# Kernel tuning notes

Measured on AMD Instinct MI355X. Metric: run time of the kernel, lower is better.

The kernel has to match this reference:

```python
import jax, jax.numpy as jnp
import numpy as np

D_MODEL = 512
N_HEADS = 8
D_K = D_MODEL // N_HEADS


def setup_inputs() -> dict:
    key = jax.random.key(0)
    ks = jax.random.split(key, 12)
    B, L = 2, 512
    s = 1.0 / np.sqrt(D_MODEL)
    sk = 1.0 / np.sqrt(D_K)
    return {
        "query": jax.random.normal(ks[0], (B, L, D_MODEL), jnp.float32),
        "key": jax.random.normal(ks[1], (B, L, D_MODEL), jnp.float32),
        "value": jax.random.normal(ks[2], (B, L, D_MODEL), jnp.float32),
        "Wq": jax.random.normal(ks[3], (D_MODEL, D_MODEL), jnp.float32) * s,
        "bq": jnp.zeros((D_MODEL,), jnp.float32),
        "Wk": jax.random.normal(ks[4], (D_MODEL, D_MODEL), jnp.float32) * s,
        "bk": jnp.zeros((D_MODEL,), jnp.float32),
        "Wv": jax.random.normal(ks[5], (D_MODEL, D_MODEL), jnp.float32) * s,
        "bv": jnp.zeros((D_MODEL,), jnp.float32),
        "Wo": jax.random.normal(ks[6], (D_MODEL, D_MODEL), jnp.float32) * s,
        "bo": jnp.zeros((D_MODEL,), jnp.float32),
        "Aq": jax.random.normal(ks[7], (D_K, D_K), jnp.float32) * sk,  # inner W_q (no bias)
        "Ak": jax.random.normal(ks[8], (D_K, D_K), jnp.float32) * sk,  # inner W_k (no bias)
        "av": jax.random.normal(ks[9], (D_K,), jnp.float32) * sk,      # inner v (d_k -> 1)
    }


def _split_heads(x):
    B, L, _ = x.shape
    return x.reshape(B, L, N_HEADS, D_K).transpose(0, 2, 1, 3)  # [B,H,L,dk]


def reference(query, key, value, Wq, bq, Wk, bk, Wv, bv, Wo, bo, Aq, Ak, av):
    # outer projections (torch Linear: x @ W.T + b)
    Q = _split_heads(query @ Wq.T + bq)   # [B,H,Lq,dk]
    K = _split_heads(key @ Wk.T + bk)     # [B,H,Lk,dk]
    V = _split_heads(value @ Wv.T + bv)   # [B,H,Lk,dk]
    # inner additive attention: e_ij = v^T tanh(Aq q_i + Ak k_j)
    qp = Q @ Aq.T                          # [B,H,Lq,dk]
    kp = K @ Ak.T                          # [B,H,Lk,dk]
    energy = jnp.tanh(qp[:, :, :, None, :] + kp[:, :, None, :, :])  # [B,H,Lq,Lk,dk]
    scores = jnp.einsum('bhqkd,d->bhqk', energy, av)
    attn = jax.nn.softmax(scores, axis=-1)  # dropout disabled (eval)
    out = jnp.einsum('bhqk,bhkd->bhqd', attn, V)  # [B,H,Lq,dk]
    B, _, Lq, _ = out.shape
    out = out.transpose(0, 2, 1, 3).reshape(B, Lq, D_MODEL)
    return out @ Wo.T + bo
```

## Files before the change

### kernel.cpp

```cpp
#include <hip/hip_runtime.h>

#define LOG2E 1.4426950408889634f

typedef __bf16 bf16x8 __attribute__((ext_vector_type(8)));
typedef float f32x4 __attribute__((ext_vector_type(4)));
typedef float f32x2 __attribute__((ext_vector_type(2)));
typedef unsigned short u16x8 __attribute__((ext_vector_type(8)));

__device__ __forceinline__ unsigned short bfb(__bf16 b){
  union { __bf16 b; unsigned short u; } z; z.b = b; return z.u;
}


__global__ __launch_bounds__(256) void prep_all(
    const float* __restrict__ Wq, const float* __restrict__ Aq,
    const float* __restrict__ Wk, const float* __restrict__ Ak,
    const float* __restrict__ bq, const float* __restrict__ bk,
    const float* __restrict__ av,
    const float* __restrict__ Wv, const float* __restrict__ Wo,
    const float* __restrict__ Qin, const float* __restrict__ Kin,
    const float* __restrict__ Vin,
    unsigned short* __restrict__ W2qp, unsigned short* __restrict__ W2kp,
    unsigned short* __restrict__ Wvp,  unsigned short* __restrict__ Wop,
    unsigned short* __restrict__ qhi, unsigned short* __restrict__ qlo,
    unsigned short* __restrict__ khi, unsigned short* __restrict__ klo,
    unsigned short* __restrict__ vhi, unsigned short* __restrict__ vlo,
    float* __restrict__ b2q, float* __restrict__ b2k, float* __restrict__ av2g){
  if (blockIdx.x >= 513){
    if (blockIdx.y) return;
    int j = blockIdx.x - 513;
    const float* src; unsigned short *dh, *dl;
    if (j < 256){ src = Qin; dh = qhi; dl = qlo; }
    else if (j < 512){ src = Kin; dh = khi; dl = klo; j -= 256; }
    else { src = Vin; dh = vhi; dl = vlo; j -= 512; }
    int base = (j * 256 + threadIdx.x) * 8;
    f32x4 v0 = *(const f32x4*)(src + base);
    f32x4 v1 = *(const f32x4*)(src + base + 4);
    u16x8 hh, ll;
    #pragma unroll
    for (int t = 0; t < 8; t++){
      float f = (t < 4) ? v0[t] : v1[t - 4];
      __bf16 hb = (__bf16)f;
      hh[t] = bfb(hb);
      ll[t] = bfb((__bf16)(f - (float)hb));
    }
    *(u16x8*)(dh + base) = hh;
    *(u16x8*)(dl + base) = ll;
    return;
  }
  if (blockIdx.x >= 256){
    if (blockIdx.x == 512){
      if (blockIdx.y == 0){
        #pragma unroll
        for (int rep = 0; rep < 2; rep++){
          int n = rep * 256 + threadIdx.x;
          int h = n >> 6, e = n & 63;
          float aq = 0.f, ak = 0.f;
          for (int c = 0; c < 64; c++){
            aq += Aq[e*64 + c] * bq[h*64 + c];
            ak += Ak[e*64 + c] * bk[h*64 + c];
          }
          b2q[n] = aq * (2.f * LOG2E);
          b2k[n] = ak * (2.f * LOG2E);
        }
      } else {
        if (threadIdx.x < 64) av2g[threadIdx.x] = -2.f * LOG2E * av[threadIdx.x];
      }
      return;
    }
    const float* src = blockIdx.y ? Wo : Wv;
    unsigned short* dst = blockIdx.y ? Wop : Wvp;
    int base = ((blockIdx.x - 256) * 256 + threadIdx.x) * 4;
    int n = base >> 9, k0 = base & 511;
    float4 v = *(const float4*)(src + base);
    ushort4 h, l;
    float f; __bf16 hb;
    f = v.x; hb = (__bf16)f; h.x = bfb(hb); l.x = bfb((__bf16)(f - (float)hb));
    f = v.y; hb = (__bf16)f; h.y = bfb(hb); l.y = bfb((__bf16)(f - (float)hb));
    f = v.z; hb = (__bf16)f; h.z = bfb(hb); l.z = bfb((__bf16)(f - (float)hb));
    f = v.w; hb = (__bf16)f; h.w = bfb(hb); l.w = bfb((__bf16)(f - (float)hb));
    int nt = n >> 4, ln = n & 15;
    int ks = k0 >> 5, q = (k0 & 31) >> 3, j0 = k0 & 7;
    size_t off = (size_t)((nt*16 + ks) * 2) * 512 + (q*16 + ln) * 8 + j0;
    *(ushort4*)(dst + off)       = h;
    *(ushort4*)(dst + off + 512) = l;
    return;
  }
  const float* W  = blockIdx.y ? Wk : Wq;
  const float* Am = blockIdx.y ? Ak : Aq;
  unsigned short* dst = blockIdx.y ? W2kp : W2qp;
  int idx = blockIdx.x * 256 + threadIdx.x;
  int n = idx >> 7;
  int k0 = (idx & 127) * 4;
  int h = n >> 6, e = n & 63;
  float4 acc = {0.f, 0.f, 0.f, 0.f};
  #pragma unroll 8
  for (int c = 0; c < 64; c++){
    float am = Am[e*64 + c];
    float4 wv = *(const float4*)(W + (size_t)(h*64 + c)*512 + k0);
    acc.x += am * wv.x;
    acc.y += am * wv.y;
    acc.z += am * wv.z;
    acc.w += am * wv.w;
  }
  int nt = n >> 4, ln = n & 15;
  int ks = k0 >> 5, q = (k0 & 31) >> 3, j0 = k0 & 7;
  size_t off = (size_t)((nt*16 + ks) * 2) * 512 + (q*16 + ln) * 8 + j0;
  ushort4 hh, ll;
  float f; __bf16 hb;
  f = acc.x * (2.f * LOG2E); hb = (__bf16)f; hh.x = bfb(hb); ll.x = bfb((__bf16)(f - (float)hb));
  f = acc.y * (2.f * LOG2E); hb = (__bf16)f; hh.y = bfb(hb); ll.y = bfb((__bf16)(f - (float)hb));
  f = acc.z * (2.f * LOG2E); hb = (__bf16)f; hh.z = bfb(hb); ll.z = bfb((__bf16)(f - (float)hb));
  f = acc.w * (2.f * LOG2E); hb = (__bf16)f; hh.w = bfb(hb); ll.w = bfb((__bf16)(f - (float)hb));
  *(ushort4*)(dst + off)       = hh;
  *(ushort4*)(dst + off + 512) = ll;
}

struct GemmBatch {
  const unsigned short* Ahi;
  const unsigned short* Alo;
  const unsigned short* Bp;
  const float* bias;
  float* Cf;
  int transposed;
  int expout;
};
struct GemmArgs { GemmBatch g[3]; };

__global__ __launch_bounds__(256) void gemm_nk(GemmArgs ga){
  GemmBatch gb = ga.g[blockIdx.z];
  __shared__ unsigned short AhiS[32 * 72];
  __shared__ unsigned short AloS[32 * 72];
  const int tid = threadIdx.x, lane = tid & 63, w = tid >> 6;
  const int l15 = lane & 15, quad = lane >> 4;
  const int m0  = blockIdx.x * 32;
  const int nt0 = blockIdx.y * 4;
  const int wr = w >> 1, wc = w & 1;
  f32x4 ac0 = {0.f,0.f,0.f,0.f}, ac1 = ac0;

  const int srow = tid >> 3;
  const int scol = (tid & 7) * 8;
  const unsigned short* srcH = gb.Ahi + (size_t)(m0 + srow) * 512 + scol;
  const unsigned short* srcL = gb.Alo + (size_t)(m0 + srow) * 512 + scol;
  unsigned short* dstH = &AhiS[srow * 72 + scol];
  unsigned short* dstL = &AloS[srow * 72 + scol];
  u16x8 ph = *(const u16x8*)srcH;
  u16x8 pl = *(const u16x8*)srcL;

  const int arow = (wr * 16 + l15) * 72;

  for (int kc = 0; kc < 8; kc++){
    __syncthreads();
    *(u16x8*)dstH = ph;
    *(u16x8*)dstL = pl;
    if (kc < 7){
      ph = *(const u16x8*)(srcH + (kc + 1) * 64);
      pl = *(const u16x8*)(srcL + (kc + 1) * 64);
    }
    __syncthreads();
    #pragma unroll
    for (int s = 0; s < 2; s++){
      int ks = kc * 2 + s;
      bf16x8 ah = *(const bf16x8*)&AhiS[arow + s*32 + quad*8];
      bf16x8 al = *(const bf16x8*)&AloS[arow + s*32 + quad*8];
      #pragma unroll
      for (int t = 0; t < 2; t++){
        int nt = nt0 + wc*2 + t;
        const unsigned short* bp = gb.Bp + (size_t)((nt*16 + ks) * 2) * 512 + lane*8;
        bf16x8 bh = *(const bf16x8*)bp;
        bf16x8 bl = *(const bf16x8*)(bp + 512);
        f32x4& ac = t ? ac1 : ac0;
        ac = __builtin_amdgcn_mfma_f32_16x16x32_bf16(ah, bh, ac, 0, 0, 0);
        ac = __builtin_amdgcn_mfma_f32_16x16x32_bf16(al, bh, ac, 0, 0, 0);
        ac = __builtin_amdgcn_mfma_f32_16x16x32_bf16(ah, bl, ac, 0, 0, 0);
      }
    }
  }

  const int mrow = m0 + wr * 16 + quad * 4;
  #pragma unroll
  for (int t = 0; t < 2; t++){
    f32x4 v = t ? ac1 : ac0;
    int n = nt0*16 + wc*32 + t*16 + l15;
    float bs = gb.bias[n];
    #pragma unroll
    for (int r = 0; r < 4; r++){
      float val = v[r] + bs;
      if (gb.expout) val = __builtin_amdgcn_exp2f(val);
      int m2 = mrow + r;
      if (gb.transposed){
        gb.Cf[(size_t)(((m2 >> 9) * 8 + (n >> 6)) * 512 + (m2 & 511)) * 64 + (n & 63)] = val;
      } else {
        gb.Cf[(size_t)m2 * 512 + n] = val;
      }
    }
  }
}

__global__ __launch_bounds__(1024, 8) void attn_kernel(
    const float* __restrict__ eqQ, const float* __restrict__ ekp,
    const float* __restrict__ Vv, const float* __restrict__ av2g,
    unsigned short* __restrict__ Ohhi, unsigned short* __restrict__ Ohlo){
  __shared__ float bufA[64 * 130];
  __shared__ float bufB[64 * 130];
  __shared__ unsigned short pcb[2 * 16 * 136];
  __shared__ float dn[16];
  __shared__ float eqs[16 * 64];
  __shared__ float avs[64];
  float* cmb = bufA;

  const int tid = threadIdx.x, lane = tid & 63, w = tid >> 6;
  const int l15 = lane & 15, quad = lane >> 4;
  const int bh = blockIdx.y;
  const int i0 = blockIdx.x * 16;
  const size_t kbase = (size_t)(bh >> 3) * 512 * 512 + (size_t)(bh & 7) * 64;
  const int r0 = __builtin_amdgcn_readfirstlane(w);
  const int ntile = w & 3, kq = w >> 2;

  float den = 0.f;
  f32x4 Cacc = {0.f, 0.f, 0.f, 0.f};

  {
    eqs[w * 64 + lane] = eqQ[((size_t)bh * 512 + i0 + w) * 64 + lane];
    if (w == 0) avs[lane] = av2g[lane];
    #pragma unroll
    for (int m = 0; m < 4; m++){
      int i = w + 16 * m;
      float a = ekp[kbase + (size_t)(2*i    ) * 512 + lane];
      float b = ekp[kbase + (size_t)(2*i + 1) * 512 + lane];
      *(float2*)&bufA[lane * 130 + 2*i] = make_float2(a, b);
    }
  }
  __syncthreads();

  for (int c = 0; c < 4; c++){
    float va[4], vb[4], ka[4], kb[4];
    #pragma unroll
    for (int m = 0; m < 4; m++){
      int i = w + 16 * m;
      va[m] = Vv[kbase + (size_t)(c*128 + 2*i    ) * 512 + lane];
      vb[m] = Vv[kbase + (size_t)(c*128 + 2*i + 1) * 512 + lane];
    }
    if (c < 3){
      #pragma unroll
      for (int m = 0; m < 4; m++){
        int i = w + 16 * m;
        ka[m] = ekp[kbase + (size_t)((c+1)*128 + 2*i    ) * 512 + lane];
        kb[m] = ekp[kbase + (size_t)((c+1)*128 + 2*i + 1) * 512 + lane];
      }
    }
    f32x2 sacc = {0.f, 0.f};
    #pragma unroll 4
    for (int d = 0; d < 64; d += 4){
      f32x4 eq4 = *(const f32x4*)&eqs[r0 * 64 + d];
      f32x4 a4  = *(const f32x4*)&avs[d];
      f32x2 ek0 = *(const f32x2*)&bufA[(d  ) * 130 + 2 * lane];
      f32x2 ek1 = *(const f32x2*)&bufA[(d+1) * 130 + 2 * lane];
      f32x2 ek2 = *(const f32x2*)&bufA[(d+2) * 130 + 2 * lane];
      f32x2 ek3 = *(const f32x2*)&bufA[(d+3) * 130 + 2 * lane];
      f32x2 A = __builtin_elementwise_fma((f32x2){eq4[0], eq4[0]}, ek0, (f32x2){1.f, 1.f});
      f32x2 B = __builtin_elementwise_fma((f32x2){eq4[1], eq4[1]}, ek1, (f32x2){1.f, 1.f});
      f32x2 t = __builtin_elementwise_fma((f32x2){a4[1], a4[1]}, A, (f32x2){a4[0], a4[0]} * B);
      f32x2 dpr = A * B;
      f32x2 r;
      r.x = __builtin_amdgcn_rcpf(dpr.x);
      r.y = __builtin_amdgcn_rcpf(dpr.y);
      sacc = __builtin_elementwise_fma(t, r, sacc);
      f32x2 C = __builtin_elementwise_fma((f32x2){eq4[2], eq4[2]}, ek2, (f32x2){1.f, 1.f});
      f32x2 D = __builtin_elementwise_fma((f32x2){eq4[3], eq4[3]}, ek3, (f32x2){1.f, 1.f});
      f32x2 t2 = __builtin_elementwise_fma((f32x2){a4[3], a4[3]}, C, (f32x2){a4[2], a4[2]} * D);
      f32x2 dpr2 = C * D;
      f32x2 r2;
      r2.x = __builtin_amdgcn_rcpf(dpr2.x);
      r2.y = __builtin_amdgcn_rcpf(dpr2.y);
      sacc = __builtin_elementwise_fma(t2, r2, sacc);
    }
    float e0 = __builtin_amdgcn_exp2f(sacc.x);
    float e1 = __builtin_amdgcn_exp2f(sacc.y);
    den += e0 + e1;
    {
      __bf16 h0 = (__bf16)e0, h1 = (__bf16)e1;
      ushort2 hi = { bfb(h0), bfb(h1) };
      ushort2 lo = { bfb((__bf16)(e0 - (float)h0)), bfb((__bf16)(e1 - (float)h1)) };
      *(ushort2*)&pcb[(0*16 + r0) * 136 + 2*lane] = hi;
      *(ushort2*)&pcb[(1*16 + r0) * 136 + 2*lane] = lo;
    }
    #pragma unroll
    for (int m = 0; m < 4; m++){
      int i = w + 16 * m;
      *(float2*)&bufB[lane * 130 + 2*i] = make_float2(va[m], vb[m]);
    }
    __syncthreads();

    {
      int k0 = kq * 32 + quad * 8;
      bf16x8 ph = *(const bf16x8*)&pcb[(0*16 + l15) * 136 + k0];
      bf16x8 pl = *(const bf16x8*)&pcb[(1*16 + l15) * 136 + k0];
      const float* vp = &bufB[(ntile*16 + l15) * 130 + k0];
      bf16x8 vh, vl;
      #pragma unroll
      for (int j = 0; j < 8; j++){
        float f = vp[j];
        __bf16 h = (__bf16)f;
        vh[j] = h; vl[j] = (__bf16)(f - (float)h);
      }
      Cacc = __builtin_amdgcn_mfma_f32_16x16x32_bf16(ph, vh, Cacc, 0, 0, 0);
      Cacc = __builtin_amdgcn_mfma_f32_16x16x32_bf16(pl, vh, Cacc, 0, 0, 0);
      Cacc = __builtin_amdgcn_mfma_f32_16x16x32_bf16(ph, vl, Cacc, 0, 0, 0);
    }
    if (c < 3){
      #pragma unroll
      for (int m = 0; m < 4; m++){
        int i = w + 16 * m;
        *(float2*)&bufA[lane * 130 + 2*i] = make_float2(ka[m], kb[m]);
      }
    }
    __syncthreads();
  }

  #pragma unroll
  for (int off = 1; off < 64; off <<= 1)
    den += __shfl_xor(den, off, 64);
  if (lane == 0) dn[r0] = den;
  if (kq > 0){
    #pragma unroll
    for (int r = 0; r < 4; r++) cmb[(w - 4) * 256 + lane * 4 + r] = Cacc[r];
  }
  __syncthreads();
  if (kq == 0){
    #pragma unroll
    for (int r = 0; r < 4; r++){
      float cv = Cacc[r];
      #pragma unroll
      for (int j = 0; j < 3; j++) cv += cmb[(j*4 + ntile) * 256 + lane * 4 + r];
      int row = quad * 4 + r;
      int d = ntile * 16 + l15;
      float val = cv / dn[row];
      __bf16 hb = (__bf16)val;
      size_t oi = kbase + (size_t)(i0 + row) * 512 + d;
      Ohhi[oi] = bfb(hb);
      Ohlo[oi] = bfb((__bf16)(val - (float)hb));
    }
  }
}

extern "C" void kernel_launch(void* const* d_in, const int* in_sizes, int n_in,
                              void* d_out, int out_size, void* d_ws, size_t ws_size,
                              hipStream_t stream){
  const float* q_in = (const float*)d_in[0];
  const float* k_in = (const float*)d_in[1];
  const float* v_in = (const float*)d_in[2];
  const float* Wq_  = (const float*)d_in[3];
  const float* bq_  = (const float*)d_in[4];
  const float* Wk_  = (const float*)d_in[5];
  const float* bk_  = (const float*)d_in[6];
  const float* Wv_  = (const float*)d_in[7];
  const float* bv_  = (const float*)d_in[8];
  const float* Wo_  = (const float*)d_in[9];
  const float* bo_  = (const float*)d_in[10];
  const float* Aq_  = (const float*)d_in[11];
  const float* Ak_  = (const float*)d_in[12];
  const float* av_  = (const float*)d_in[13];

  char* ws = (char*)d_ws;
  unsigned short* W2qp = (unsigned short*)(ws + 0);
  unsigned short* W2kp = (unsigned short*)(ws + 1048576);
  unsigned short* Ohhi = (unsigned short*)(ws + 0);
  unsigned short* Ohlo = (unsigned short*)(ws + 1048576);
  unsigned short* Wvp  = (unsigned short*)(ws + 2097152);
  unsigned short* Wop  = (unsigned short*)(ws + 3145728);
  float* b2q  = (float*)(ws + 4194304);
  float* b2k  = (float*)(ws + 4196352);
  float* av2g = (float*)(ws + 4198400);
  float* eqQ  = (float*)(ws + 4198656);
  float* ekp  = (float*)(ws + 6295808);
  float* Vw   = (float*)(ws + 8392960);
  unsigned short* qhi = (unsigned short*)(ws + 10490112);
  unsigned short* qlo = (unsigned short*)(ws + 11538688);
  unsigned short* khi = (unsigned short*)(ws + 12587264);
  unsigned short* klo = (unsigned short*)(ws + 13635840);
  unsigned short* vhi = (unsigned short*)(ws + 14684416);
  unsigned short* vlo = (unsigned short*)(ws + 15732992);

  prep_all<<<dim3(1281, 2, 1), 256, 0, stream>>>(Wq_, Aq_, Wk_, Ak_, bq_, bk_, av_,
                                                 Wv_, Wo_, q_in, k_in, v_in,
                                                 W2qp, W2kp, Wvp, Wop,
                                                 qhi, qlo, khi, klo, vhi, vlo,
                                                 b2q, b2k, av2g);

  GemmArgs ga;
  ga.g[0] = { qhi, qlo, W2qp, b2q, eqQ, 1, 1 };
  ga.g[1] = { khi, klo, W2kp, b2k, ekp, 0, 1 };
  ga.g[2] = { vhi, vlo, Wvp,  bv_, Vw,  0, 0 };
  gemm_nk<<<dim3(32, 8, 3), 256, 0, stream>>>(ga);

  attn_kernel<<<dim3(32, 16, 1), 1024, 0, stream>>>(eqQ, ekp, Vw, av2g, Ohhi, Ohlo);

  GemmArgs go;
  go.g[0] = { Ohhi, Ohlo, Wop, bo_, (float*)d_out, 0, 0 };
  go.g[1] = go.g[0];
  go.g[2] = go.g[0];
  gemm_nk<<<dim3(32, 8, 1), 256, 0, stream>>>(go);
}
```

Baseline: 151.8 us.

## Split attention over key blocks with atomic accumulation and register-tiled scores

Replaces the single-pass attention kernel (one block of 1024 threads per 16 query rows, looping over all keys) with a split-K kernel. Each 256-thread block handles 64 queries by 128 keys and keeps 16 query rows per wave in registers, so each key element loaded from shared memory is reused across rows. Partial P·V results and softmax denominators are accumulated into global buffers with atomicAdd, and a new finish kernel normalises the output and converts it to split bf16. The V projection GEMM now writes V pre-transposed and pre-split into bf16 hi/lo, and prep_all zeroes the accumulators. This adds an extra launch and atomic traffic, and the summation order is no longer deterministic.

```diff
diff --git a/kernel.cpp b/kernel.cpp
--- a/kernel.cpp
+++ b/kernel.cpp
@@ -25,9 +25,19 @@
     unsigned short* __restrict__ qhi, unsigned short* __restrict__ qlo,
     unsigned short* __restrict__ khi, unsigned short* __restrict__ klo,
     unsigned short* __restrict__ vhi, unsigned short* __restrict__ vlo,
-    float* __restrict__ b2q, float* __restrict__ b2k, float* __restrict__ av2g){
+    float* __restrict__ b2q, float* __restrict__ b2k, float* __restrict__ av2g,
+    float* __restrict__ zbase){
   if (blockIdx.x >= 513){
-    if (blockIdx.y) return;
+    if (blockIdx.y){
+      int x = blockIdx.x - 513;
+      if (x < 260){
+        float* z = zbase + (size_t)(x * 256 + threadIdx.x) * 8;
+        f32x4 zz = {0.f, 0.f, 0.f, 0.f};
+        *(f32x4*)z = zz;
+        *(f32x4*)(z + 4) = zz;
+      }
+      return;
+    }
     int j = blockIdx.x - 513;
     const float* src; unsigned short *dh, *dl;
     if (j < 256){ src = Qin; dh = qhi; dl = qlo; }
@@ -122,8 +132,11 @@
   const unsigned short* Bp;
   const float* bias;
   float* Cf;
+  unsigned short* Chi;
+  unsigned short* Clo;
   int transposed;
   int expout;
+  int dual;
 };
 struct GemmArgs { GemmBatch g[3]; };
 
@@ -188,7 +201,12 @@
       float val = v[r] + bs;
       if (gb.expout) val = __builtin_amdgcn_exp2f(val);
       int m2 = mrow + r;
-      if (gb.transposed){
+      if (gb.dual){
+        size_t o = (size_t)(((m2 >> 9) * 8 + (n >> 6)) * 64 + (n & 63)) * 512 + (m2 & 511);
+        __bf16 hb = (__bf16)val;
+        gb.Chi[o] = bfb(hb);
+        gb.Clo[o] = bfb((__bf16)(val - (float)hb));
+      } else if (gb.transposed){
         gb.Cf[(size_t)(((m2 >> 9) * 8 + (n >> 6)) * 512 + (m2 & 511)) * 64 + (n & 63)] = val;
       } else {
         gb.Cf[(size_t)m2 * 512 + n] = val;
@@ -197,67 +215,56 @@
   }
 }
 
-__global__ __launch_bounds__(1024, 8) void attn_kernel(
+__global__ __launch_bounds__(256, 3) void score_pv(
     const float* __restrict__ eqQ, const float* __restrict__ ekp,
-    const float* __restrict__ Vv, const float* __restrict__ av2g,
-    unsigned short* __restrict__ Ohhi, unsigned short* __restrict__ Ohlo){
-  __shared__ float bufA[64 * 130];
-  __shared__ float bufB[64 * 130];
-  __shared__ unsigned short pcb[2 * 16 * 136];
-  __shared__ float dn[16];
-  __shared__ float eqs[16 * 64];
-  __shared__ float avs[64];
-  float* cmb = bufA;
+    const float* __restrict__ av2g,
+    const unsigned short* __restrict__ vthi, const unsigned short* __restrict__ vtlo,
+    float* __restrict__ Og, float* __restrict__ deng){
+  __shared__ float SHf[12480];
+  float* EKt = SHf;
+  float* EQs = SHf + 8320;
+  float* avS = SHf + 12416;
+  unsigned short* Ph = (unsigned short*)SHf;
+  unsigned short* Pl = (unsigned short*)SHf + 8704;
 
   const int tid = threadIdx.x, lane = tid & 63, w = tid >> 6;
   const int l15 = lane & 15, quad = lane >> 4;
-  const int bh = blockIdx.y;
-  const int i0 = blockIdx.x * 16;
-  const size_t kbase = (size_t)(bh >> 3) * 512 * 512 + (size_t)(bh & 7) * 64;
-  const int r0 = __builtin_amdgcn_readfirstlane(w);
-  const int ntile = w & 3, kq = w >> 2;
-
-  float den = 0.f;
-  f32x4 Cacc = {0.f, 0.f, 0.f, 0.f};
+  const int bh = blockIdx.z, b = bh >> 3, h = bh & 7;
+  const int i0 = blockIdx.y * 64;
+  const int j0 = blockIdx.x * 128;
 
   {
-    eqs[w * 64 + lane] = eqQ[((size_t)bh * 512 + i0 + w) * 64 + lane];
-    if (w == 0) avs[lane] = av2g[lane];
-    #pragma unroll
-    for (int m = 0; m < 4; m++){
-      int i = w + 16 * m;
-      float a = ekp[kbase + (size_t)(2*i    ) * 512 + lane];
-      float b = ekp[kbase + (size_t)(2*i + 1) * 512 + lane];
-      *(float2*)&bufA[lane * 130 + 2*i] = make_float2(a, b);
+    int r = tid >> 2, c = (tid & 3) * 16;
+    const float* s = eqQ + ((size_t)bh * 512 + i0 + r) * 64 + c;
+    #pragma unroll
+    for (int u = 0; u < 4; u++)
+      *(f32x4*)&EQs[r * 64 + c + u * 4] = *(const f32x4*)(s + u * 4);
+  }
+  if (tid < 64) avS[tid] = av2g[tid];
+  {
+    int j = tid >> 1, c0 = (tid & 1) * 32;
+    const float* s = ekp + ((size_t)(b * 512) + j0 + j) * 512 + h * 64 + c0;
+    #pragma unroll
+    for (int u = 0; u < 8; u++){
+      f32x4 v = *(const f32x4*)(s + u * 4);
+      #pragma unroll
+      for (int q = 0; q < 4; q++) EKt[(c0 + u * 4 + q) * 130 + j] = v[q];
     }
   }
   __syncthreads();
 
-  for (int c = 0; c < 4; c++){
-    float va[4], vb[4], ka[4], kb[4];
-    #pragma unroll
-    for (int m = 0; m < 4; m++){
-      int i = w + 16 * m;
-      va[m] = Vv[kbase + (size_t)(c*128 + 2*i    ) * 512 + lane];
-      vb[m] = Vv[kbase + (size_t)(c*128 + 2*i + 1) * 512 + lane];
-    }
-    if (c < 3){
-      #pragma unroll
-      for (int m = 0; m < 4; m++){
-        int i = w + 16 * m;
-        ka[m] = ekp[kbase + (size_t)((c+1)*128 + 2*i    ) * 512 + lane];
-        kb[m] = ekp[kbase + (size_t)((c+1)*128 + 2*i + 1) * 512 + lane];
-      }
-    }
-    f32x2 sacc = {0.f, 0.f};
-    #pragma unroll 4
-    for (int d = 0; d < 64; d += 4){
-      f32x4 eq4 = *(const f32x4*)&eqs[r0 * 64 + d];
-      f32x4 a4  = *(const f32x4*)&avs[d];
-      f32x2 ek0 = *(const f32x2*)&bufA[(d  ) * 130 + 2 * lane];
-      f32x2 ek1 = *(const f32x2*)&bufA[(d+1) * 130 + 2 * lane];
-      f32x2 ek2 = *(const f32x2*)&bufA[(d+2) * 130 + 2 * lane];
-      f32x2 ek3 = *(const f32x2*)&bufA[(d+3) * 130 + 2 * lane];
+  f32x2 acc[16];
+  #pragma unroll
+  for (int ii = 0; ii < 16; ii++) acc[ii] = (f32x2){0.f, 0.f};
+  for (int d = 0; d < 64; d += 4){
+    f32x2 ek0 = *(const f32x2*)&EKt[(d    ) * 130 + 2 * lane];
+    f32x2 ek1 = *(const f32x2*)&EKt[(d + 1) * 130 + 2 * lane];
+    f32x2 ek2 = *(const f32x2*)&EKt[(d + 2) * 130 + 2 * lane];
+    f32x2 ek3 = *(const f32x2*)&EKt[(d + 3) * 130 + 2 * lane];
+    f32x4 a4 = *(const f32x4*)&avS[d];
+    #pragma unroll
+    for (int ii = 0; ii < 16; ii++){
+      f32x4 eq4 = *(const f32x4*)&EQs[(w * 16 + ii) * 64 + d];
       f32x2 A = __builtin_elementwise_fma((f32x2){eq4[0], eq4[0]}, ek0, (f32x2){1.f, 1.f});
       f32x2 B = __builtin_elementwise_fma((f32x2){eq4[1], eq4[1]}, ek1, (f32x2){1.f, 1.f});
       f32x2 t = __builtin_elementwise_fma((f32x2){a4[1], a4[1]}, A, (f32x2){a4[0], a4[0]} * B);
@@ -265,7 +272,7 @@
       f32x2 r;
       r.x = __builtin_amdgcn_rcpf(dpr.x);
       r.y = __builtin_amdgcn_rcpf(dpr.y);
-      sacc = __builtin_elementwise_fma(t, r, sacc);
+      acc[ii] = __builtin_elementwise_fma(t, r, acc[ii]);
       f32x2 C = __builtin_elementwise_fma((f32x2){eq4[2], eq4[2]}, ek2, (f32x2){1.f, 1.f});
       f32x2 D = __builtin_elementwise_fma((f32x2){eq4[3], eq4[3]}, ek3, (f32x2){1.f, 1.f});
       f32x2 t2 = __builtin_elementwise_fma((f32x2){a4[3], a4[3]}, C, (f32x2){a4[2], a4[2]} * D);
@@ -273,75 +280,80 @@
       f32x2 r2;
       r2.x = __builtin_amdgcn_rcpf(dpr2.x);
       r2.y = __builtin_amdgcn_rcpf(dpr2.y);
-      sacc = __builtin_elementwise_fma(t2, r2, sacc);
-    }
-    float e0 = __builtin_amdgcn_exp2f(sacc.x);
-    float e1 = __builtin_amdgcn_exp2f(sacc.y);
-    den += e0 + e1;
-    {
-      __bf16 h0 = (__bf16)e0, h1 = (__bf16)e1;
-      ushort2 hi = { bfb(h0), bfb(h1) };
-      ushort2 lo = { bfb((__bf16)(e0 - (float)h0)), bfb((__bf16)(e1 - (float)h1)) };
-      *(ushort2*)&pcb[(0*16 + r0) * 136 + 2*lane] = hi;
-      *(ushort2*)&pcb[(1*16 + r0) * 136 + 2*lane] = lo;
-    }
-    #pragma unroll
-    for (int m = 0; m < 4; m++){
-      int i = w + 16 * m;
-      *(float2*)&bufB[lane * 130 + 2*i] = make_float2(va[m], vb[m]);
-    }
-    __syncthreads();
-
-    {
-      int k0 = kq * 32 + quad * 8;
-      bf16x8 ph = *(const bf16x8*)&pcb[(0*16 + l15) * 136 + k0];
-      bf16x8 pl = *(const bf16x8*)&pcb[(1*16 + l15) * 136 + k0];
-      const float* vp = &bufB[(ntile*16 + l15) * 130 + k0];
-      bf16x8 vh, vl;
-      #pragma unroll
-      for (int j = 0; j < 8; j++){
-        float f = vp[j];
-        __bf16 h = (__bf16)f;
-        vh[j] = h; vl[j] = (__bf16)(f - (float)h);
-      }
-      Cacc = __builtin_amdgcn_mfma_f32_16x16x32_bf16(ph, vh, Cacc, 0, 0, 0);
-      Cacc = __builtin_amdgcn_mfma_f32_16x16x32_bf16(pl, vh, Cacc, 0, 0, 0);
-      Cacc = __builtin_amdgcn_mfma_f32_16x16x32_bf16(ph, vl, Cacc, 0, 0, 0);
-    }
-    if (c < 3){
-      #pragma unroll
-      for (int m = 0; m < 4; m++){
-        int i = w + 16 * m;
-        *(float2*)&bufA[lane * 130 + 2*i] = make_float2(ka[m], kb[m]);
-      }
-    }
-    __syncthreads();
-  }
-
-  #pragma unroll
-  for (int off = 1; off < 64; off <<= 1)
-    den += __shfl_xor(den, off, 64);
-  if (lane == 0) dn[r0] = den;
-  if (kq > 0){
-    #pragma unroll
-    for (int r = 0; r < 4; r++) cmb[(w - 4) * 256 + lane * 4 + r] = Cacc[r];
+      acc[ii] = __builtin_elementwise_fma(t2, r2, acc[ii]);
+    }
+  }
+  #pragma unroll
+  for (int ii = 0; ii < 16; ii++){
+    acc[ii].x = __builtin_amdgcn_exp2f(acc[ii].x);
+    acc[ii].y = __builtin_amdgcn_exp2f(acc[ii].y);
   }
   __syncthreads();
-  if (kq == 0){
+  #pragma unroll
+  for (int ii = 0; ii < 16; ii++){
+    float s2 = acc[ii].x + acc[ii].y;
+    #pragma unroll
+    for (int off = 1; off < 64; off <<= 1) s2 += __shfl_xor(s2, off, 64);
+    if (lane == 0) atomicAdd(&deng[bh * 512 + i0 + w * 16 + ii], s2);
+    __bf16 h0 = (__bf16)acc[ii].x, h1 = (__bf16)acc[ii].y;
+    ushort2 hi = { bfb(h0), bfb(h1) };
+    ushort2 lo = { bfb((__bf16)(acc[ii].x - (float)h0)), bfb((__bf16)(acc[ii].y - (float)h1)) };
+    *(ushort2*)&Ph[(w * 16 + ii) * 136 + 2 * lane] = hi;
+    *(ushort2*)&Pl[(w * 16 + ii) * 136 + 2 * lane] = lo;
+  }
+  __syncthreads();
+
+  f32x4 o0 = {0.f,0.f,0.f,0.f}, o1 = o0, o2 = o0, o3 = o0;
+  const size_t vbase = ((size_t)bh * 64) * 512 + j0;
+  #pragma unroll
+  for (int ks = 0; ks < 4; ks++){
+    bf16x8 pa = *(const bf16x8*)&Ph[(w * 16 + l15) * 136 + ks * 32 + quad * 8];
+    bf16x8 pb = *(const bf16x8*)&Pl[(w * 16 + l15) * 136 + ks * 32 + quad * 8];
+    #pragma unroll
+    for (int nt = 0; nt < 4; nt++){
+      size_t vo = vbase + (size_t)(nt * 16 + l15) * 512 + ks * 32 + quad * 8;
+      bf16x8 vh = *(const bf16x8*)(vthi + vo);
+      bf16x8 vl = *(const bf16x8*)(vtlo + vo);
+      f32x4& o = nt == 0 ? o0 : nt == 1 ? o1 : nt == 2 ? o2 : o3;
+      o = __builtin_amdgcn_mfma_f32_16x16x32_bf16(pa, vh, o, 0, 0, 0);
+      o = __builtin_amdgcn_mfma_f32_16x16x32_bf16(pb, vh, o, 0, 0, 0);
+      o = __builtin_amdgcn_mfma_f32_16x16x32_bf16(pa, vl, o, 0, 0, 0);
+    }
+  }
+  #pragma unroll
+  for (int nt = 0; nt < 4; nt++){
+    f32x4 o = nt == 0 ? o0 : nt == 1 ? o1 : nt == 2 ? o2 : o3;
+    int d = nt * 16 + l15;
     #pragma unroll
     for (int r = 0; r < 4; r++){
-      float cv = Cacc[r];
-      #pragma unroll
-      for (int j = 0; j < 3; j++) cv += cmb[(j*4 + ntile) * 256 + lane * 4 + r];
-      int row = quad * 4 + r;
-      int d = ntile * 16 + l15;
-      float val = cv / dn[row];
-      __bf16 hb = (__bf16)val;
-      size_t oi = kbase + (size_t)(i0 + row) * 512 + d;
-      Ohhi[oi] = bfb(hb);
-      Ohlo[oi] = bfb((__bf16)(val - (float)hb));
-    }
-  }
+      int i = i0 + w * 16 + quad * 4 + r;
+      atomicAdd(&Og[((size_t)bh * 512 + i) * 64 + d], o[r]);
+    }
+  }
+}
+
+__global__ __launch_bounds__(256) void finish_oh(
+    const float* __restrict__ Og, const float* __restrict__ deng,
+    unsigned short* __restrict__ Ohhi, unsigned short* __restrict__ Ohlo){
+  int t = blockIdx.x * 256 + threadIdx.x;
+  int bh = t >> 12;
+  int i  = (t >> 3) & 511;
+  int d0 = (t & 7) * 8;
+  float rv = 1.0f / deng[bh * 512 + i];
+  const float* src = Og + ((size_t)bh * 512 + i) * 64 + d0;
+  f32x4 v0 = *(const f32x4*)src;
+  f32x4 v1 = *(const f32x4*)(src + 4);
+  u16x8 hh, ll;
+  #pragma unroll
+  for (int u = 0; u < 8; u++){
+    float f = ((u < 4) ? v0[u] : v1[u - 4]) * rv;
+    __bf16 hb = (__bf16)f;
+    hh[u] = bfb(hb);
+    ll[u] = bfb((__bf16)(f - (float)hb));
+  }
+  size_t o = ((size_t)(bh >> 3) * 512 + i) * 512 + (bh & 7) * 64 + d0;
+  *(u16x8*)(Ohhi + o) = hh;
+  *(u16x8*)(Ohlo + o) = ll;
 }
 
 extern "C" void kernel_launch(void* const* d_in, const int* in_sizes, int n_in,
@@ -374,30 +386,35 @@
   float* av2g = (float*)(ws + 4198400);
   float* eqQ  = (float*)(ws + 4198656);
   float* ekp  = (float*)(ws + 6295808);
-  float* Vw   = (float*)(ws + 8392960);
+  unsigned short* vthi = (unsigned short*)(ws + 8392960);
+  unsigned short* vtlo = (unsigned short*)(ws + 9441536);
   unsigned short* qhi = (unsigned short*)(ws + 10490112);
   unsigned short* qlo = (unsigned short*)(ws + 11538688);
   unsigned short* khi = (unsigned short*)(ws + 12587264);
   unsigned short* klo = (unsigned short*)(ws + 13635840);
   unsigned short* vhi = (unsigned short*)(ws + 14684416);
   unsigned short* vlo = (unsigned short*)(ws + 15732992);
+  float* deng = (float*)(ws + 16781568);
+  float* Og   = (float*)(ws + 16814336);
 
   prep_all<<<dim3(1281, 2, 1), 256, 0, stream>>>(Wq_, Aq_, Wk_, Ak_, bq_, bk_, av_,
                                                  Wv_, Wo_, q_in, k_in, v_in,
                                                  W2qp, W2kp, Wvp, Wop,
                                                  qhi, qlo, khi, klo, vhi, vlo,
-                                                 b2q, b2k, av2g);
+                                                 b2q, b2k, av2g, deng);
 
   GemmArgs ga;
-  ga.g[0] = { qhi, qlo, W2qp, b2q, eqQ, 1, 1 };
-  ga.g[1] = { khi, klo, W2kp, b2k, ekp, 0, 1 };
-  ga.g[2] = { vhi, vlo, Wvp,  bv_, Vw,  0, 0 };
+  ga.g[0] = { qhi, qlo, W2qp, b2q, eqQ, 0, 0, 1, 1, 0 };
+  ga.g[1] = { khi, klo, W2kp, b2k, ekp, 0, 0, 0, 1, 0 };
+  ga.g[2] = { vhi, vlo, Wvp,  bv_, 0, vthi, vtlo, 0, 0, 1 };
   gemm_nk<<<dim3(32, 8, 3), 256, 0, stream>>>(ga);
 
-  attn_kernel<<<dim3(32, 16, 1), 1024, 0, stream>>>(eqQ, ekp, Vw, av2g, Ohhi, Ohlo);
+  score_pv<<<dim3(4, 8, 16), 256, 0, stream>>>(eqQ, ekp, av2g, vthi, vtlo, Og, deng);
+
+  finish_oh<<<dim3(256, 1, 1), 256, 0, stream>>>(Og, deng, Ohhi, Ohlo);
 
   GemmArgs go;
-  go.g[0] = { Ohhi, Ohlo, Wop, bo_, (float*)d_out, 0, 0 };
+  go.g[0] = { Ohhi, Ohlo, Wop, bo_, (float*)d_out, 0, 0, 0, 0, 0 };
   go.g[1] = go.g[0];
   go.g[2] = go.g[0];
   gemm_nk<<<dim3(32, 8, 1), 256, 0, stream>>>(go);
```

After: 163.6 us. 7.7% more time.

## Emit transposed K and pre-split bf16 V from projection GEMM, drop attention LDS staging

Applied to the files above, without the earlier changes.

The projection GEMM gains transposed epilogues that go through shared memory. It writes exp-transformed K in a d-major per-head layout and V as transposed bf16 hi/lo pairs. The attention kernel then reads K directly from global memory with contiguous per-lane loads and reads V fragments already split into bf16. This removes the two large LDS staging buffers, the register prefetch and LDS write steps, and the per-block fp32-to-bf16 splitting of V, which was repeated by every query block. In exchange, each wave issues global loads inside the inner tanh loop and depends on cache hits, and the GEMM epilogue gains an extra shared-memory round trip.

```diff
diff --git a/kernel.cpp b/kernel.cpp
--- a/kernel.cpp
+++ b/kernel.cpp
@@ -122,15 +122,19 @@
   const unsigned short* Bp;
   const float* bias;
   float* Cf;
+  unsigned short* Chi;
+  unsigned short* Clo;
   int transposed;
   int expout;
+  int dual;
 };
 struct GemmArgs { GemmBatch g[3]; };
 
 __global__ __launch_bounds__(256) void gemm_nk(GemmArgs ga){
   GemmBatch gb = ga.g[blockIdx.z];
-  __shared__ unsigned short AhiS[32 * 72];
-  __shared__ unsigned short AloS[32 * 72];
+  __shared__ unsigned short AhiS[64 * 40];
+  __shared__ unsigned short AloS[64 * 40];
+  __shared__ float TfS[64 * 40];
   const int tid = threadIdx.x, lane = tid & 63, w = tid >> 6;
   const int l15 = lane & 15, quad = lane >> 4;
   const int m0  = blockIdx.x * 32;
@@ -177,6 +181,57 @@
     }
   }
 
+  if (gb.dual){
+    __syncthreads();
+    #pragma unroll
+    for (int t = 0; t < 2; t++){
+      f32x4 v = t ? ac1 : ac0;
+      int nl = wc*32 + t*16 + l15;
+      float bs = gb.bias[nt0*16 + nl];
+      #pragma unroll
+      for (int r = 0; r < 4; r++){
+        float val = v[r] + bs;
+        int ml = wr*16 + quad*4 + r;
+        __bf16 hb = (__bf16)val;
+        AhiS[nl*40 + ml] = bfb(hb);
+        AloS[nl*40 + ml] = bfb((__bf16)(val - (float)hb));
+      }
+    }
+    __syncthreads();
+    int nl = tid >> 2, mq = (tid & 3) * 8;
+    int hh2 = (nt0 * 16) >> 6;
+    int b2 = m0 >> 9;
+    size_t o = (size_t)((b2*8 + hh2)*64 + ((nt0*16 + nl) & 63)) * 512 + (m0 & 511) + mq;
+    *(u16x8*)(gb.Chi + o) = *(const u16x8*)&AhiS[nl*40 + mq];
+    *(u16x8*)(gb.Clo + o) = *(const u16x8*)&AloS[nl*40 + mq];
+    return;
+  }
+
+  if (gb.transposed == 2){
+    __syncthreads();
+    #pragma unroll
+    for (int t = 0; t < 2; t++){
+      f32x4 v = t ? ac1 : ac0;
+      int nl = wc*32 + t*16 + l15;
+      float bs = gb.bias[nt0*16 + nl];
+      #pragma unroll
+      for (int r = 0; r < 4; r++){
+        float val = v[r] + bs;
+        if (gb.expout) val = __builtin_amdgcn_exp2f(val);
+        int ml = wr*16 + quad*4 + r;
+        TfS[nl*40 + ml] = val;
+      }
+    }
+    __syncthreads();
+    int nl = tid >> 2, mq = (tid & 3) * 8;
+    int hh2 = (nt0 * 16) >> 6;
+    int b2 = m0 >> 9;
+    size_t o = (size_t)((b2*8 + hh2)*64 + ((nt0*16 + nl) & 63)) * 512 + (m0 & 511) + mq;
+    *(f32x4*)(gb.Cf + o)     = *(const f32x4*)&TfS[nl*40 + mq];
+    *(f32x4*)(gb.Cf + o + 4) = *(const f32x4*)&TfS[nl*40 + mq + 4];
+    return;
+  }
+
   const int mrow = m0 + wr * 16 + quad * 4;
   #pragma unroll
   for (int t = 0; t < 2; t++){
@@ -198,66 +253,43 @@
 }
 
 __global__ __launch_bounds__(1024, 8) void attn_kernel(
-    const float* __restrict__ eqQ, const float* __restrict__ ekp,
-    const float* __restrict__ Vv, const float* __restrict__ av2g,
+    const float* __restrict__ eqQ, const float* __restrict__ ekT,
+    const float* __restrict__ av2g,
+    const unsigned short* __restrict__ vthi, const unsigned short* __restrict__ vtlo,
     unsigned short* __restrict__ Ohhi, unsigned short* __restrict__ Ohlo){
-  __shared__ float bufA[64 * 130];
-  __shared__ float bufB[64 * 130];
   __shared__ unsigned short pcb[2 * 16 * 136];
   __shared__ float dn[16];
   __shared__ float eqs[16 * 64];
   __shared__ float avs[64];
-  float* cmb = bufA;
+  __shared__ float cmb[12 * 256];
 
   const int tid = threadIdx.x, lane = tid & 63, w = tid >> 6;
   const int l15 = lane & 15, quad = lane >> 4;
   const int bh = blockIdx.y;
   const int i0 = blockIdx.x * 16;
-  const size_t kbase = (size_t)(bh >> 3) * 512 * 512 + (size_t)(bh & 7) * 64;
   const int r0 = __builtin_amdgcn_readfirstlane(w);
   const int ntile = w & 3, kq = w >> 2;
+  const size_t ebase = (size_t)bh * 64 * 512;
+  const size_t obase = (size_t)(bh >> 3) * 512 * 512 + (size_t)(bh & 7) * 64;
 
   float den = 0.f;
   f32x4 Cacc = {0.f, 0.f, 0.f, 0.f};
 
-  {
-    eqs[w * 64 + lane] = eqQ[((size_t)bh * 512 + i0 + w) * 64 + lane];
-    if (w == 0) avs[lane] = av2g[lane];
-    #pragma unroll
-    for (int m = 0; m < 4; m++){
-      int i = w + 16 * m;
-      float a = ekp[kbase + (size_t)(2*i    ) * 512 + lane];
-      float b = ekp[kbase + (size_t)(2*i + 1) * 512 + lane];
-      *(float2*)&bufA[lane * 130 + 2*i] = make_float2(a, b);
-    }
-  }
+  eqs[w * 64 + lane] = eqQ[((size_t)bh * 512 + i0 + w) * 64 + lane];
+  if (w == 0) avs[lane] = av2g[lane];
   __syncthreads();
 
   for (int c = 0; c < 4; c++){
-    float va[4], vb[4], ka[4], kb[4];
-    #pragma unroll
-    for (int m = 0; m < 4; m++){
-      int i = w + 16 * m;
-      va[m] = Vv[kbase + (size_t)(c*128 + 2*i    ) * 512 + lane];
-      vb[m] = Vv[kbase + (size_t)(c*128 + 2*i + 1) * 512 + lane];
-    }
-    if (c < 3){
-      #pragma unroll
-      for (int m = 0; m < 4; m++){
-        int i = w + 16 * m;
-        ka[m] = ekp[kbase + (size_t)((c+1)*128 + 2*i    ) * 512 + lane];
-        kb[m] = ekp[kbase + (size_t)((c+1)*128 + 2*i + 1) * 512 + lane];
-      }
-    }
+    const float* ekc = ekT + ebase + c * 128 + 2 * lane;
     f32x2 sacc = {0.f, 0.f};
     #pragma unroll 4
     for (int d = 0; d < 64; d += 4){
       f32x4 eq4 = *(const f32x4*)&eqs[r0 * 64 + d];
       f32x4 a4  = *(const f32x4*)&avs[d];
-      f32x2 ek0 = *(const f32x2*)&bufA[(d  ) * 130 + 2 * lane];
-      f32x2 ek1 = *(const f32x2*)&bufA[(d+1) * 130 + 2 * lane];
-      f32x2 ek2 = *(const f32x2*)&bufA[(d+2) * 130 + 2 * lane];
-      f32x2 ek3 = *(const f32x2*)&bufA[(d+3) * 130 + 2 * lane];
+      f32x2 ek0 = *(const f32x2*)(ekc + (size_t)(d    ) * 512);
+      f32x2 ek1 = *(const f32x2*)(ekc + (size_t)(d + 1) * 512);
+      f32x2 ek2 = *(const f32x2*)(ekc + (size_t)(d + 2) * 512);
+      f32x2 ek3 = *(const f32x2*)(ekc + (size_t)(d + 3) * 512);
       f32x2 A = __builtin_elementwise_fma((f32x2){eq4[0], eq4[0]}, ek0, (f32x2){1.f, 1.f});
       f32x2 B = __builtin_elementwise_fma((f32x2){eq4[1], eq4[1]}, ek1, (f32x2){1.f, 1.f});
       f32x2 t = __builtin_elementwise_fma((f32x2){a4[1], a4[1]}, A, (f32x2){a4[0], a4[0]} * B);
@@ -285,35 +317,18 @@
       *(ushort2*)&pcb[(0*16 + r0) * 136 + 2*lane] = hi;
       *(ushort2*)&pcb[(1*16 + r0) * 136 + 2*lane] = lo;
     }
-    #pragma unroll
-    for (int m = 0; m < 4; m++){
-      int i = w + 16 * m;
-      *(float2*)&bufB[lane * 130 + 2*i] = make_float2(va[m], vb[m]);
-    }
     __syncthreads();
 
     {
       int k0 = kq * 32 + quad * 8;
       bf16x8 ph = *(const bf16x8*)&pcb[(0*16 + l15) * 136 + k0];
       bf16x8 pl = *(const bf16x8*)&pcb[(1*16 + l15) * 136 + k0];
-      const float* vp = &bufB[(ntile*16 + l15) * 130 + k0];
-      bf16x8 vh, vl;
-      #pragma unroll
-      for (int j = 0; j < 8; j++){
-        float f = vp[j];
-        __bf16 h = (__bf16)f;
-        vh[j] = h; vl[j] = (__bf16)(f - (float)h);
-      }
+      size_t vo = ebase + (size_t)(ntile * 16 + l15) * 512 + c * 128 + k0;
+      bf16x8 vh = *(const bf16x8*)(vthi + vo);
+      bf16x8 vl = *(const bf16x8*)(vtlo + vo);
       Cacc = __builtin_amdgcn_mfma_f32_16x16x32_bf16(ph, vh, Cacc, 0, 0, 0);
       Cacc = __builtin_amdgcn_mfma_f32_16x16x32_bf16(pl, vh, Cacc, 0, 0, 0);
       Cacc = __builtin_amdgcn_mfma_f32_16x16x32_bf16(ph, vl, Cacc, 0, 0, 0);
-    }
-    if (c < 3){
-      #pragma unroll
-      for (int m = 0; m < 4; m++){
-        int i = w + 16 * m;
-        *(float2*)&bufA[lane * 130 + 2*i] = make_float2(ka[m], kb[m]);
-      }
     }
     __syncthreads();
   }
@@ -337,7 +352,7 @@
       int d = ntile * 16 + l15;
       float val = cv / dn[row];
       __bf16 hb = (__bf16)val;
-      size_t oi = kbase + (size_t)(i0 + row) * 512 + d;
+      size_t oi = obase + (size_t)(i0 + row) * 512 + d;
       Ohhi[oi] = bfb(hb);
       Ohlo[oi] = bfb((__bf16)(val - (float)hb));
     }
@@ -373,8 +388,9 @@
   float* b2k  = (float*)(ws + 4196352);
   float* av2g = (float*)(ws + 4198400);
   float* eqQ  = (float*)(ws + 4198656);
-  float* ekp  = (float*)(ws + 6295808);
-  float* Vw   = (float*)(ws + 8392960);
+  float* ekT  = (float*)(ws + 6295808);
+  unsigned short* vthi = (unsigned short*)(ws + 8392960);
+  unsigned short* vtlo = (unsigned short*)(ws + 9441536);
   unsigned short* qhi = (unsigned short*)(ws + 10490112);
   unsigned short* qlo = (unsigned short*)(ws + 11538688);
   unsigned short* khi = (unsigned short*)(ws + 12587264);
@@ -389,15 +405,15 @@
                                                  b2q, b2k, av2g);
 
   GemmArgs ga;
-  ga.g[0] = { qhi, qlo, W2qp, b2q, eqQ, 1, 1 };
-  ga.g[1] = { khi, klo, W2kp, b2k, ekp, 0, 1 };
-  ga.g[2] = { vhi, vlo, Wvp,  bv_, Vw,  0, 0 };
+  ga.g[0] = { qhi, qlo, W2qp, b2q, eqQ, 0, 0, 1, 1, 0 };
+  ga.g[1] = { khi, klo, W2kp, b2k, ekT, 0, 0, 2, 1, 0 };
+  ga.g[2] = { vhi, vlo, Wvp,  bv_, 0, vthi, vtlo, 0, 0, 1 };
   gemm_nk<<<dim3(32, 8, 3), 256, 0, stream>>>(ga);
 
-  attn_kernel<<<dim3(32, 16, 1), 1024, 0, stream>>>(eqQ, ekp, Vw, av2g, Ohhi, Ohlo);
+  attn_kernel<<<dim3(32, 16, 1), 1024, 0, stream>>>(eqQ, ekT, av2g, vthi, vtlo, Ohhi, Ohlo);
 
   GemmArgs go;
-  go.g[0] = { Ohhi, Ohlo, Wop, bo_, (float*)d_out, 0, 0 };
+  go.g[0] = { Ohhi, Ohlo, Wop, bo_, (float*)d_out, 0, 0, 0, 0, 0 };
   go.g[1] = go.g[0];
   go.g[2] = go.g[0];
   gemm_nk<<<dim3(32, 8, 1), 256, 0, stream>>>(go);
```

Result: slower. 191.9 us (+26.4%).

## Process two query rows per wave in attention kernel to reuse key tiles

Applied to the files above, without the earlier changes.

Each workgroup now covers 32 query rows instead of 16, and each wave computes additive-attention scores for two query rows, so every LDS read of the key tile is reused twice. The PV MFMA stage is reorganised so waves split over row tile, column tile and two k-halves, with a simpler two-way reduction at the end. This halves the grid size and the repeated K/V global loads per query row. In exchange it raises register pressure (launch bounds relaxed to 4) and cuts the number of blocks available to fill the GPU.

```diff
diff --git a/kernel.cpp b/kernel.cpp
--- a/kernel.cpp
+++ b/kernel.cpp
@@ -197,31 +197,32 @@
   }
 }
 
-__global__ __launch_bounds__(1024, 8) void attn_kernel(
+__global__ __launch_bounds__(1024, 4) void attn_kernel(
     const float* __restrict__ eqQ, const float* __restrict__ ekp,
     const float* __restrict__ Vv, const float* __restrict__ av2g,
     unsigned short* __restrict__ Ohhi, unsigned short* __restrict__ Ohlo){
   __shared__ float bufA[64 * 130];
   __shared__ float bufB[64 * 130];
-  __shared__ unsigned short pcb[2 * 16 * 136];
-  __shared__ float dn[16];
-  __shared__ float eqs[16 * 64];
+  __shared__ unsigned short pcb[2 * 32 * 136];
+  __shared__ float dn[32];
+  __shared__ float eqs[32 * 64];
   __shared__ float avs[64];
   float* cmb = bufA;
 
   const int tid = threadIdx.x, lane = tid & 63, w = tid >> 6;
   const int l15 = lane & 15, quad = lane >> 4;
   const int bh = blockIdx.y;
-  const int i0 = blockIdx.x * 16;
+  const int i0 = blockIdx.x * 32;
   const size_t kbase = (size_t)(bh >> 3) * 512 * 512 + (size_t)(bh & 7) * 64;
-  const int r0 = __builtin_amdgcn_readfirstlane(w);
-  const int ntile = w & 3, kq = w >> 2;
-
-  float den = 0.f;
+  const int r0 = __builtin_amdgcn_readfirstlane(2 * w);
+  const int rt = w >> 3, nt4 = (w >> 1) & 3, kq = w & 1;
+
+  float den0 = 0.f, den1 = 0.f;
   f32x4 Cacc = {0.f, 0.f, 0.f, 0.f};
 
   {
-    eqs[w * 64 + lane] = eqQ[((size_t)bh * 512 + i0 + w) * 64 + lane];
+    eqs[(2*w    ) * 64 + lane] = eqQ[((size_t)bh * 512 + i0 + 2*w    ) * 64 + lane];
+    eqs[(2*w + 1) * 64 + lane] = eqQ[((size_t)bh * 512 + i0 + 2*w + 1) * 64 + lane];
     if (w == 0) avs[lane] = av2g[lane];
     #pragma unroll
     for (int m = 0; m < 4; m++){
@@ -249,41 +250,69 @@
         kb[m] = ekp[kbase + (size_t)((c+1)*128 + 2*i + 1) * 512 + lane];
       }
     }
-    f32x2 sacc = {0.f, 0.f};
+    f32x2 sacc0 = {0.f, 0.f}, sacc1 = {0.f, 0.f};
     #pragma unroll 4
     for (int d = 0; d < 64; d += 4){
-      f32x4 eq4 = *(const f32x4*)&eqs[r0 * 64 + d];
+      f32x4 eqa = *(const f32x4*)&eqs[(r0    ) * 64 + d];
+      f32x4 eqb = *(const f32x4*)&eqs[(r0 + 1) * 64 + d];
       f32x4 a4  = *(const f32x4*)&avs[d];
       f32x2 ek0 = *(const f32x2*)&bufA[(d  ) * 130 + 2 * lane];
       f32x2 ek1 = *(const f32x2*)&bufA[(d+1) * 130 + 2 * lane];
       f32x2 ek2 = *(const f32x2*)&bufA[(d+2) * 130 + 2 * lane];
       f32x2 ek3 = *(const f32x2*)&bufA[(d+3) * 130 + 2 * lane];
-      f32x2 A = __builtin_elementwise_fma((f32x2){eq4[0], eq4[0]}, ek0, (f32x2){1.f, 1.f});
-      f32x2 B = __builtin_elementwise_fma((f32x2){eq4[1], eq4[1]}, ek1, (f32x2){1.f, 1.f});
-      f32x2 t = __builtin_elementwise_fma((f32x2){a4[1], a4[1]}, A, (f32x2){a4[0], a4[0]} * B);
-      f32x2 dpr = A * B;
-      f32x2 r;
-      r.x = __builtin_amdgcn_rcpf(dpr.x);
-      r.y = __builtin_amdgcn_rcpf(dpr.y);
-      sacc = __builtin_elementwise_fma(t, r, sacc);
-      f32x2 C = __builtin_elementwise_fma((f32x2){eq4[2], eq4[2]}, ek2, (f32x2){1.f, 1.f});
-      f32x2 D = __builtin_elementwise_fma((f32x2){eq4[3], eq4[3]}, ek3, (f32x2){1.f, 1.f});
-      f32x2 t2 = __builtin_elementwise_fma((f32x2){a4[3], a4[3]}, C, (f32x2){a4[2], a4[2]} * D);
-      f32x2 dpr2 = C * D;
-      f32x2 r2;
-      r2.x = __builtin_amdgcn_rcpf(dpr2.x);
-      r2.y = __builtin_amdgcn_rcpf(dpr2.y);
-      sacc = __builtin_elementwise_fma(t2, r2, sacc);
-    }
-    float e0 = __builtin_amdgcn_exp2f(sacc.x);
-    float e1 = __builtin_amdgcn_exp2f(sacc.y);
-    den += e0 + e1;
+      {
+        f32x2 A = __builtin_elementwise_fma((f32x2){eqa[0], eqa[0]}, ek0, (f32x2){1.f, 1.f});
+        f32x2 B = __builtin_elementwise_fma((f32x2){eqa[1], eqa[1]}, ek1, (f32x2){1.f, 1.f});
+        f32x2 t = __builtin_elementwise_fma((f32x2){a4[1], a4[1]}, A, (f32x2){a4[0], a4[0]} * B);
+        f32x2 dpr = A * B;
+        f32x2 r;
+        r.x = __builtin_amdgcn_rcpf(dpr.x);
+        r.y = __builtin_amdgcn_rcpf(dpr.y);
+        sacc0 = __builtin_elementwise_fma(t, r, sacc0);
+        f32x2 C = __builtin_elementwise_fma((f32x2){eqa[2], eqa[2]}, ek2, (f32x2){1.f, 1.f});
+        f32x2 D = __builtin_elementwise_fma((f32x2){eqa[3], eqa[3]}, ek3, (f32x2){1.f, 1.f});
+        f32x2 t2 = __builtin_elementwise_fma((f32x2){a4[3], a4[3]}, C, (f32x2){a4[2], a4[2]} * D);
+        f32x2 dpr2 = C * D;
+        f32x2 r2;
+        r2.x = __builtin_amdgcn_rcpf(dpr2.x);
+        r2.y = __builtin_amdgcn_rcpf(dpr2.y);
+        sacc0 = __builtin_elementwise_fma(t2, r2, sacc0);
+      }
+      {
+        f32x2 A = __builtin_elementwise_fma((f32x2){eqb[0], eqb[0]}, ek0, (f32x2){1.f, 1.f});
+        f32x2 B = __builtin_elementwise_fma((f32x2){eqb[1], eqb[1]}, ek1, (f32x2){1.f, 1.f});
+        f32x2 t = __builtin_elementwise_fma((f32x2){a4[1], a4[1]}, A, (f32x2){a4[0], a4[0]} * B);
+        f32x2 dpr = A * B;
+        f32x2 r;
+        r.x = __builtin_amdgcn_rcpf(dpr.x);
+        r.y = __builtin_amdgcn_rcpf(dpr.y);
+        sacc1 = __builtin_elementwise_fma(t, r, sacc1);
+        f32x2 C = __builtin_elementwise_fma((f32x2){eqb[2], eqb[2]}, ek2, (f32x2){1.f, 1.f});
+        f32x2 D = __builtin_elementwise_fma((f32x2){eqb[3], eqb[3]}, ek3, (f32x2){1.f, 1.f});
+        f32x2 t2 = __builtin_elementwise_fma((f32x2){a4[3], a4[3]}, C, (f32x2){a4[2], a4[2]} * D);
+        f32x2 dpr2 = C * D;
+        f32x2 r2;
+        r2.x = __builtin_amdgcn_rcpf(dpr2.x);
+        r2.y = __builtin_amdgcn_rcpf(dpr2.y);
+        sacc1 = __builtin_elementwise_fma(t2, r2, sacc1);
+      }
+    }
+    float e00 = __builtin_amdgcn_exp2f(sacc0.x);
+    float e01 = __builtin_amdgcn_exp2f(sacc0.y);
+    float e10 = __builtin_amdgcn_exp2f(sacc1.x);
+    float e11 = __builtin_amdgcn_exp2f(sacc1.y);
+    den0 += e00 + e01;
+    den1 += e10 + e11;
     {
-      __bf16 h0 = (__bf16)e0, h1 = (__bf16)e1;
-      ushort2 hi = { bfb(h0), bfb(h1) };
-      ushort2 lo = { bfb((__bf16)(e0 - (float)h0)), bfb((__bf16)(e1 - (float)h1)) };
-      *(ushort2*)&pcb[(0*16 + r0) * 136 + 2*lane] = hi;
-      *(ushort2*)&pcb[(1*16 + r0) * 136 + 2*lane] = lo;
+      __bf16 h00 = (__bf16)e00, h01 = (__bf16)e01, h10 = (__bf16)e10, h11 = (__bf16)e11;
+      ushort2 hi0 = { bfb(h00), bfb(h01) };
+      ushort2 hi1 = { bfb(h10), bfb(h11) };
+      ushort2 lo0 = { bfb((__bf16)(e00 - (float)h00)), bfb((__bf16)(e01 - (float)h01)) };
+      ushort2 lo1 = { bfb((__bf16)(e10 - (float)h10)), bfb((__bf16)(e11 - (float)h11)) };
+      *(ushort2*)&pcb[(0*32 + r0    ) * 136 + 2*lane] = hi0;
+      *(ushort2*)&pcb[(0*32 + r0 + 1) * 136 + 2*lane] = hi1;
+      *(ushort2*)&pcb[(1*32 + r0    ) * 136 + 2*lane] = lo0;
+      *(ushort2*)&pcb[(1*32 + r0 + 1) * 136 + 2*lane] = lo1;
     }
     #pragma unroll
     for (int m = 0; m < 4; m++){
@@ -292,11 +321,12 @@
     }
     __syncthreads();
 
-    {
-      int k0 = kq * 32 + quad * 8;
-      bf16x8 ph = *(const bf16x8*)&pcb[(0*16 + l15) * 136 + k0];
-      bf16x8 pl = *(const bf16x8*)&pcb[(1*16 + l15) * 136 + k0];
-      const float* vp = &bufB[(ntile*16 + l15) * 130 + k0];
+    #pragma unroll
+    for (int ks = 0; ks < 2; ks++){
+      int k0 = kq * 64 + ks * 32 + quad * 8;
+      bf16x8 ph = *(const bf16x8*)&pcb[(0*32 + rt*16 + l15) * 136 + k0];
+      bf16x8 pl = *(const bf16x8*)&pcb[(1*32 + rt*16 + l15) * 136 + k0];
+      const float* vp = &bufB[(nt4*16 + l15) * 130 + k0];
       bf16x8 vh, vl;
       #pragma unroll
       for (int j = 0; j < 8; j++){
@@ -319,22 +349,22 @@
   }
 
   #pragma unroll
-  for (int off = 1; off < 64; off <<= 1)
-    den += __shfl_xor(den, off, 64);
-  if (lane == 0) dn[r0] = den;
-  if (kq > 0){
-    #pragma unroll
-    for (int r = 0; r < 4; r++) cmb[(w - 4) * 256 + lane * 4 + r] = Cacc[r];
+  for (int off = 1; off < 64; off <<= 1){
+    den0 += __shfl_xor(den0, off, 64);
+    den1 += __shfl_xor(den1, off, 64);
+  }
+  if (lane == 0){ dn[r0] = den0; dn[r0 + 1] = den1; }
+  if (kq == 1){
+    #pragma unroll
+    for (int r = 0; r < 4; r++) cmb[(rt*4 + nt4) * 256 + lane * 4 + r] = Cacc[r];
   }
   __syncthreads();
   if (kq == 0){
     #pragma unroll
     for (int r = 0; r < 4; r++){
-      float cv = Cacc[r];
-      #pragma unroll
-      for (int j = 0; j < 3; j++) cv += cmb[(j*4 + ntile) * 256 + lane * 4 + r];
-      int row = quad * 4 + r;
-      int d = ntile * 16 + l15;
+      float cv = Cacc[r] + cmb[(rt*4 + nt4) * 256 + lane * 4 + r];
+      int row = rt * 16 + quad * 4 + r;
+      int d = nt4 * 16 + l15;
       float val = cv / dn[row];
       __bf16 hb = (__bf16)val;
       size_t oi = kbase + (size_t)(i0 + row) * 512 + d;
@@ -394,7 +424,7 @@
   ga.g[2] = { vhi, vlo, Wvp,  bv_, Vw,  0, 0 };
   gemm_nk<<<dim3(32, 8, 3), 256, 0, stream>>>(ga);
 
-  attn_kernel<<<dim3(32, 16, 1), 1024, 0, stream>>>(eqQ, ekp, Vw, av2g, Ohhi, Ohlo);
+  attn_kernel<<<dim3(16, 16, 1), 1024, 0, stream>>>(eqQ, ekp, Vw, av2g, Ohhi, Ohlo);
 
   GemmArgs go;
   go.g[0] = { Ohhi, Ohlo, Wop, bo_, (float*)d_out, 0, 0 };
```

Result: no change. 150.1 us (-1.2%).
